# Kernel tuning notes

Hardware: AMD Instinct MI355X
Metric: run time of the kernel (lower is better)

The kernel has to match this reference:

```python
import jax, jax.numpy as jnp
import numpy as np

HEAD_DIM = 32
KERNEL = 3
DILATION = 2
SCALE = HEAD_DIM ** -0.5


def _unfold(x, kernel, dilation):
    # x: [B, C, H, W] -> patches [B, C, kernel*kernel, H, W]
    # matches nn.Unfold(kernel, dilation, padding=dilation*(kernel-1)//2, stride=1)
    B, C, H, W = x.shape
    pad = dilation * (kernel - 1) // 2
    xp = jnp.pad(x, ((0, 0), (0, 0), (pad, pad), (pad, pad)))
    patches = jnp.stack(
        [xp[:, :, i * dilation:i * dilation + H, j * dilation:j * dilation + W]
         for i in range(kernel) for j in range(kernel)],
        axis=2,
    )
    return patches  # [B, C, k*k, H, W]


def setup_inputs() -> dict:
    key = jax.random.key(0)
    kq, kk, kv = jax.random.split(key, 3)
    shape = (8, 192, 56, 56)
    return {
        "q": jax.random.normal(kq, shape, dtype=jnp.float32),
        "k": jax.random.normal(kk, shape, dtype=jnp.float32),
        "v": jax.random.normal(kv, shape, dtype=jnp.float32),
    }


def reference(q, k, v):
    B, d, H, W = q.shape
    h = d // HEAD_DIM
    kk2 = KERNEL * KERNEL
    HW = H * W

    # q: [B, h, hd, HW]
    qh = q.reshape(B, h, HEAD_DIM, HW)
    # unfolded k/v: [B, h, hd, k*k, HW]
    kp = _unfold(k, KERNEL, DILATION).reshape(B, h, HEAD_DIM, kk2, HW)
    vp = _unfold(v, KERNEL, DILATION).reshape(B, h, HEAD_DIM, kk2, HW)

    attn = jnp.einsum('bhdn,bhdkn->bhnk', qh, kp) * SCALE
    attn = jax.nn.softmax(attn, axis=-1)
    # dropout p=0 (eval): no-op

    # [B, h, HW, hd]
    out = jnp.einsum('bhnk,bhdkn->bhnd', attn, vp)
    # transpose(1,2).reshape(B,H,W,d): channel order = head-major
    out = out.transpose(0, 2, 1, 3).reshape(B, H, W, d)
    return out
```

## Files before the change

### kernel.cpp

```cpp
#include <hip/hip_runtime.h>

#define BATCH 8
#define NH 6
#define HEAD_DIM 32
#define CCH 192
#define HH 56
#define WW 56
#define HWSZ (HH * WW)
#define KPOS 9
#define SCALE 0.17677669529663687f

__global__ __launch_bounds__(256) void dilate_attn_kernel(
    const float* __restrict__ q,
    const float* __restrict__ k,
    const float* __restrict__ v,
    float* __restrict__ out)
{
    int tid = blockIdx.x * blockDim.x + threadIdx.x;
    if (tid >= BATCH * NH * HWSZ) return;

    int x  = tid % WW;
    int y  = (tid / WW) % HH;
    int bh = tid / HWSZ;
    int h  = bh % NH;
    int b  = bh / NH;

    const size_t chan_base = (size_t)(b * CCH + h * HEAD_DIM) * HWSZ;
    const float* qb = q + chan_base + y * WW + x;
    const float* kb = k + chan_base;
    const float* vb = v + chan_base;

    int  off[KPOS];
    bool ok[KPOS];
#pragma unroll
    for (int kk = 0; kk < KPOS; kk++) {
        int yy = y + 2 * (kk / 3) - 2;
        int xx = x + 2 * (kk % 3) - 2;
        bool good = (yy >= 0) & (yy < HH) & (xx >= 0) & (xx < WW);
        ok[kk]  = good;
        off[kk] = good ? (yy * WW + xx) : 0;
    }

    float attn[KPOS];
#pragma unroll
    for (int kk = 0; kk < KPOS; kk++) attn[kk] = 0.0f;

#pragma unroll 4
    for (int d = 0; d < HEAD_DIM; d++) {
        float qd = qb[(size_t)d * HWSZ];
        const float* kd = kb + (size_t)d * HWSZ;
#pragma unroll
        for (int kk = 0; kk < KPOS; kk++) {
            float kval = ok[kk] ? kd[off[kk]] : 0.0f;
            attn[kk] = fmaf(qd, kval, attn[kk]);
        }
    }

    float m = attn[0] * SCALE;
#pragma unroll
    for (int kk = 0; kk < KPOS; kk++) {
        attn[kk] *= SCALE;
        m = fmaxf(m, attn[kk]);
    }
    float s = 0.0f;
#pragma unroll
    for (int kk = 0; kk < KPOS; kk++) {
        attn[kk] = __expf(attn[kk] - m);
        s += attn[kk];
    }
    float inv = 1.0f / s;
#pragma unroll
    for (int kk = 0; kk < KPOS; kk++) attn[kk] *= inv;

    float* ob = out + ((size_t)((b * HH + y) * WW + x)) * CCH + h * HEAD_DIM;

#pragma unroll 2
    for (int d4 = 0; d4 < HEAD_DIM; d4 += 4) {
        float4 acc = make_float4(0.f, 0.f, 0.f, 0.f);
        const float* vd = vb + (size_t)d4 * HWSZ;
#pragma unroll
        for (int kk = 0; kk < KPOS; kk++) {
            if (ok[kk]) {
                const float* vp = vd + off[kk];
                acc.x = fmaf(attn[kk], vp[0 * HWSZ], acc.x);
                acc.y = fmaf(attn[kk], vp[1 * HWSZ], acc.y);
                acc.z = fmaf(attn[kk], vp[2 * HWSZ], acc.z);
                acc.w = fmaf(attn[kk], vp[3 * HWSZ], acc.w);
            }
        }
        *reinterpret_cast<float4*>(ob + d4) = acc;
    }
}

extern "C" void kernel_launch(void* const* d_in, const int* in_sizes, int n_in,
                              void* d_out, int out_size, void* d_ws, size_t ws_size,
                              hipStream_t stream) {
    const float* q = (const float*)d_in[0];
    const float* k = (const float*)d_in[1];
    const float* v = (const float*)d_in[2];
    float* out = (float*)d_out;

    const int total = BATCH * NH * HWSZ;
    const int block = 256;
    const int grid  = (total + block - 1) / block;
    dilate_attn_kernel<<<grid, block, 0, stream>>>(q, k, v, out);
}
```

Before: 129.3 us.

## Repack K/V into zero-padded channel-last planes and vectorize tap loads

Adds a repack kernel that transposes K and V into a zero-padded [bh, 60, 60, 32] channel-last layout in workspace. The main kernel can then read each tap's 32 channels as contiguous float4 loads without bounds checks. It also preloads q into registers. This replaces strided per-channel gathers with vectorized loads, at the cost of an extra kernel launch and a full write and reread of K and V through global memory.

```diff
diff --git a/kernel.cpp b/kernel.cpp
--- a/kernel.cpp
+++ b/kernel.cpp
@@ -7,61 +7,96 @@
 #define HH 56
 #define WW 56
 #define HWSZ (HH * WW)
+#define PH 60
+#define PW 60
+#define PPLANE (PH * PW)
 #define KPOS 9
 #define SCALE 0.17677669529663687f
 
-__global__ __launch_bounds__(256) void dilate_attn_kernel(
+__global__ __launch_bounds__(256) void repack_kernel(
+    const float* __restrict__ k, const float* __restrict__ v,
+    float* __restrict__ kp, float* __restrict__ vp)
+{
+    __shared__ float lds[HEAD_DIM * 57];
+
+    int yy = blockIdx.x % PH;
+    int bh = blockIdx.x / PH;
+    const float* src = (blockIdx.y == 0) ? k : v;
+    float*       dst = (blockIdx.y == 0) ? kp : vp;
+
+    int t = threadIdx.x;
+    bool interior_row = (yy >= 2) && (yy < 58);
+
+    if (interior_row) {
+        int y = yy - 2;
+        const float* s = src + (size_t)bh * (HEAD_DIM * HWSZ) + y * WW;
+#pragma unroll
+        for (int i = 0; i < 7; i++) {
+            int idx = t + i * 256;
+            int d = idx / WW;
+            int x = idx - d * WW;
+            lds[d * 57 + x] = s[d * HWSZ + x];
+        }
+    }
+    __syncthreads();
+
+    float* drow = dst + ((size_t)bh * PPLANE + (size_t)yy * PW) * HEAD_DIM;
+#pragma unroll
+    for (int i = 0; i < 8; i++) {
+        int idx = t + i * 256;
+        if (idx < PW * HEAD_DIM) {
+            int xx = idx >> 5;
+            int d  = idx & 31;
+            float val = 0.0f;
+            if (interior_row && xx >= 2 && xx < 58)
+                val = lds[d * 57 + (xx - 2)];
+            drow[idx] = val;
+        }
+    }
+}
+
+__global__ __launch_bounds__(256) void dilate_attn_main(
     const float* __restrict__ q,
-    const float* __restrict__ k,
-    const float* __restrict__ v,
+    const float* __restrict__ kp,
+    const float* __restrict__ vp,
     float* __restrict__ out)
 {
-    int tid = blockIdx.x * blockDim.x + threadIdx.x;
-    if (tid >= BATCH * NH * HWSZ) return;
-
+    int tid = blockIdx.x * 256 + threadIdx.x;
     int x  = tid % WW;
     int y  = (tid / WW) % HH;
     int bh = tid / HWSZ;
-    int h  = bh % NH;
-    int b  = bh / NH;
 
-    const size_t chan_base = (size_t)(b * CCH + h * HEAD_DIM) * HWSZ;
-    const float* qb = q + chan_base + y * WW + x;
-    const float* kb = k + chan_base;
-    const float* vb = v + chan_base;
+    const float* qb = q + (size_t)bh * (HEAD_DIM * HWSZ) + y * WW + x;
+    float qreg[HEAD_DIM];
+#pragma unroll
+    for (int d = 0; d < HEAD_DIM; d++) qreg[d] = qb[d * HWSZ];
 
-    int  off[KPOS];
-    bool ok[KPOS];
+    int tap[KPOS];
 #pragma unroll
     for (int kk = 0; kk < KPOS; kk++) {
-        int yy = y + 2 * (kk / 3) - 2;
-        int xx = x + 2 * (kk % 3) - 2;
-        bool good = (yy >= 0) & (yy < HH) & (xx >= 0) & (xx < WW);
-        ok[kk]  = good;
-        off[kk] = good ? (yy * WW + xx) : 0;
+        int iy = kk / 3, ix = kk % 3;
+        tap[kk] = (bh * PPLANE + (y + 2 * iy) * PW + (x + 2 * ix)) * HEAD_DIM;
     }
 
     float attn[KPOS];
 #pragma unroll
-    for (int kk = 0; kk < KPOS; kk++) attn[kk] = 0.0f;
-
-#pragma unroll 4
-    for (int d = 0; d < HEAD_DIM; d++) {
-        float qd = qb[(size_t)d * HWSZ];
-        const float* kd = kb + (size_t)d * HWSZ;
+    for (int kk = 0; kk < KPOS; kk++) {
+        const float4* kt = reinterpret_cast<const float4*>(kp + tap[kk]);
+        float acc = 0.0f;
 #pragma unroll
-        for (int kk = 0; kk < KPOS; kk++) {
-            float kval = ok[kk] ? kd[off[kk]] : 0.0f;
-            attn[kk] = fmaf(qd, kval, attn[kk]);
+        for (int j = 0; j < 8; j++) {
+            float4 kv = kt[j];
+            acc = fmaf(qreg[4 * j + 0], kv.x, acc);
+            acc = fmaf(qreg[4 * j + 1], kv.y, acc);
+            acc = fmaf(qreg[4 * j + 2], kv.z, acc);
+            acc = fmaf(qreg[4 * j + 3], kv.w, acc);
         }
+        attn[kk] = acc * SCALE;
     }
 
-    float m = attn[0] * SCALE;
+    float m = attn[0];
 #pragma unroll
-    for (int kk = 0; kk < KPOS; kk++) {
-        attn[kk] *= SCALE;
-        m = fmaxf(m, attn[kk]);
-    }
+    for (int kk = 1; kk < KPOS; kk++) m = fmaxf(m, attn[kk]);
     float s = 0.0f;
 #pragma unroll
     for (int kk = 0; kk < KPOS; kk++) {
@@ -72,24 +107,30 @@
 #pragma unroll
     for (int kk = 0; kk < KPOS; kk++) attn[kk] *= inv;
 
+    float4 acc[8];
+#pragma unroll
+    for (int j = 0; j < 8; j++) acc[j] = make_float4(0.f, 0.f, 0.f, 0.f);
+
+#pragma unroll
+    for (int kk = 0; kk < KPOS; kk++) {
+        const float4* vt = reinterpret_cast<const float4*>(vp + tap[kk]);
+        float a = attn[kk];
+#pragma unroll
+        for (int j = 0; j < 8; j++) {
+            float4 vv = vt[j];
+            acc[j].x = fmaf(a, vv.x, acc[j].x);
+            acc[j].y = fmaf(a, vv.y, acc[j].y);
+            acc[j].z = fmaf(a, vv.z, acc[j].z);
+            acc[j].w = fmaf(a, vv.w, acc[j].w);
+        }
+    }
+
+    int h = bh % NH;
+    int b = bh / NH;
     float* ob = out + ((size_t)((b * HH + y) * WW + x)) * CCH + h * HEAD_DIM;
-
-#pragma unroll 2
-    for (int d4 = 0; d4 < HEAD_DIM; d4 += 4) {
-        float4 acc = make_float4(0.f, 0.f, 0.f, 0.f);
-        const float* vd = vb + (size_t)d4 * HWSZ;
+    float4* ob4 = reinterpret_cast<float4*>(ob);
 #pragma unroll
-        for (int kk = 0; kk < KPOS; kk++) {
-            if (ok[kk]) {
-                const float* vp = vd + off[kk];
-                acc.x = fmaf(attn[kk], vp[0 * HWSZ], acc.x);
-                acc.y = fmaf(attn[kk], vp[1 * HWSZ], acc.y);
-                acc.z = fmaf(attn[kk], vp[2 * HWSZ], acc.z);
-                acc.w = fmaf(attn[kk], vp[3 * HWSZ], acc.w);
-            }
-        }
-        *reinterpret_cast<float4*>(ob + d4) = acc;
-    }
+    for (int j = 0; j < 8; j++) ob4[j] = acc[j];
 }
 
 extern "C" void kernel_launch(void* const* d_in, const int* in_sizes, int n_in,
@@ -100,8 +141,13 @@
     const float* v = (const float*)d_in[2];
     float* out = (float*)d_out;
 
+    const size_t plane_elems = (size_t)BATCH * NH * PPLANE * HEAD_DIM;
+    float* kp = (float*)d_ws;
+    float* vp = kp + plane_elems;
+
+    dim3 rgrid(BATCH * NH * PH, 2);
+    repack_kernel<<<rgrid, 256, 0, stream>>>(k, v, kp, vp);
+
     const int total = BATCH * NH * HWSZ;
-    const int block = 256;
-    const int grid  = (total + block - 1) / block;
-    dilate_attn_kernel<<<grid, block, 0, stream>>>(q, k, v, out);
+    dilate_attn_main<<<total / 256, 256, 0, stream>>>(q, kp, vp, out);
 }
```

After: 184.1 us. 42.5% more time.

## Split QK and AV phases across threads with shared-memory attention weights

Applied to the files above, without the earlier changes.

Each block now handles 64 pixels with 256 threads. In the first phase, threads are assigned per pixel and kernel row (3 rows, so 192 active threads), and each computes three dot products. The resulting scores go to shared memory. In the second phase, 4 threads per pixel each compute softmax and accumulate 8 output channels over the 9 neighbours. This raises parallelism per pixel and spreads the V gathers and stores across more threads, which helps latency hiding. The cost is a block barrier, a quarter of threads idle in phase one, and softmax computed redundantly by all four threads of each pixel.

```diff
diff --git a/kernel.cpp b/kernel.cpp
--- a/kernel.cpp
+++ b/kernel.cpp
@@ -1,6 +1,5 @@
 #include <hip/hip_runtime.h>
 
-#define BATCH 8
 #define NH 6
 #define HEAD_DIM 32
 #define CCH 192
@@ -9,86 +8,105 @@
 #define HWSZ (HH * WW)
 #define KPOS 9
 #define SCALE 0.17677669529663687f
+#define PXB 64
 
-__global__ __launch_bounds__(256) void dilate_attn_kernel(
+__global__ __launch_bounds__(256) void dilate_attn_fused(
     const float* __restrict__ q,
     const float* __restrict__ k,
     const float* __restrict__ v,
     float* __restrict__ out)
 {
-    int tid = blockIdx.x * blockDim.x + threadIdx.x;
-    if (tid >= BATCH * NH * HWSZ) return;
+    __shared__ float sattn[PXB * 13];
+    const int t = threadIdx.x;
 
-    int x  = tid % WW;
-    int y  = (tid / WW) % HH;
-    int bh = tid / HWSZ;
-    int h  = bh % NH;
-    int b  = bh / NH;
+    {
+        const int iy = t >> 6;
+        const int pl = t & 63;
+        if (iy < 3) {
+            const int gp = blockIdx.x * PXB + pl;
+            const int x  = gp % WW;
+            const int y  = (gp / WW) % HH;
+            const int bh = gp / HWSZ;
+            const int yy = y + 2 * iy - 2;
 
-    const size_t chan_base = (size_t)(b * CCH + h * HEAD_DIM) * HWSZ;
-    const float* qb = q + chan_base + y * WW + x;
-    const float* kb = k + chan_base;
-    const float* vb = v + chan_base;
-
-    int  off[KPOS];
-    bool ok[KPOS];
+            float a0 = 0.f, a1 = 0.f, a2 = 0.f;
+            if (yy >= 0 && yy < HH) {
+                const float* qb = q + (size_t)bh * (HEAD_DIM * HWSZ) + y * WW + x;
+                const float* kb = k + (size_t)bh * (HEAD_DIM * HWSZ) + yy * WW;
+                const bool ok0 = (x - 2) >= 0;
+                const bool ok2 = (x + 2) < WW;
+                const int  o0  = ok0 ? (x - 2) : 0;
+                const int  o1  = x;
+                const int  o2  = ok2 ? (x + 2) : 0;
 #pragma unroll
-    for (int kk = 0; kk < KPOS; kk++) {
-        int yy = y + 2 * (kk / 3) - 2;
-        int xx = x + 2 * (kk % 3) - 2;
-        bool good = (yy >= 0) & (yy < HH) & (xx >= 0) & (xx < WW);
-        ok[kk]  = good;
-        off[kk] = good ? (yy * WW + xx) : 0;
-    }
-
-    float attn[KPOS];
-#pragma unroll
-    for (int kk = 0; kk < KPOS; kk++) attn[kk] = 0.0f;
-
-#pragma unroll 4
-    for (int d = 0; d < HEAD_DIM; d++) {
-        float qd = qb[(size_t)d * HWSZ];
-        const float* kd = kb + (size_t)d * HWSZ;
-#pragma unroll
-        for (int kk = 0; kk < KPOS; kk++) {
-            float kval = ok[kk] ? kd[off[kk]] : 0.0f;
-            attn[kk] = fmaf(qd, kval, attn[kk]);
+                for (int d = 0; d < HEAD_DIM; d++) {
+                    const float qd = qb[d * HWSZ];
+                    const float* kd = kb + d * HWSZ;
+                    a0 = fmaf(qd, kd[o0], a0);
+                    a1 = fmaf(qd, kd[o1], a1);
+                    a2 = fmaf(qd, kd[o2], a2);
+                }
+                if (!ok0) a0 = 0.f;
+                if (!ok2) a2 = 0.f;
+            }
+            sattn[pl * 13 + iy * 3 + 0] = a0 * SCALE;
+            sattn[pl * 13 + iy * 3 + 1] = a1 * SCALE;
+            sattn[pl * 13 + iy * 3 + 2] = a2 * SCALE;
         }
     }
 
-    float m = attn[0] * SCALE;
+    __syncthreads();
+
+    {
+        const int pl = t >> 2;
+        const int dq = t & 3;
+        const int gp = blockIdx.x * PXB + pl;
+        const int x  = gp % WW;
+        const int y  = (gp / WW) % HH;
+        const int bh = gp / HWSZ;
+
+        float a[KPOS];
 #pragma unroll
-    for (int kk = 0; kk < KPOS; kk++) {
-        attn[kk] *= SCALE;
-        m = fmaxf(m, attn[kk]);
-    }
-    float s = 0.0f;
+        for (int kk = 0; kk < KPOS; kk++) a[kk] = sattn[pl * 13 + kk];
+
+        float m = a[0];
 #pragma unroll
-    for (int kk = 0; kk < KPOS; kk++) {
-        attn[kk] = __expf(attn[kk] - m);
-        s += attn[kk];
-    }
-    float inv = 1.0f / s;
-#pragma unroll
-    for (int kk = 0; kk < KPOS; kk++) attn[kk] *= inv;
-
-    float* ob = out + ((size_t)((b * HH + y) * WW + x)) * CCH + h * HEAD_DIM;
-
-#pragma unroll 2
-    for (int d4 = 0; d4 < HEAD_DIM; d4 += 4) {
-        float4 acc = make_float4(0.f, 0.f, 0.f, 0.f);
-        const float* vd = vb + (size_t)d4 * HWSZ;
+        for (int kk = 1; kk < KPOS; kk++) m = fmaxf(m, a[kk]);
+        float s = 0.f;
 #pragma unroll
         for (int kk = 0; kk < KPOS; kk++) {
-            if (ok[kk]) {
-                const float* vp = vd + off[kk];
-                acc.x = fmaf(attn[kk], vp[0 * HWSZ], acc.x);
-                acc.y = fmaf(attn[kk], vp[1 * HWSZ], acc.y);
-                acc.z = fmaf(attn[kk], vp[2 * HWSZ], acc.z);
-                acc.w = fmaf(attn[kk], vp[3 * HWSZ], acc.w);
-            }
+            a[kk] = __expf(a[kk] - m);
+            s += a[kk];
         }
-        *reinterpret_cast<float4*>(ob + d4) = acc;
+        const float inv = 1.f / s;
+
+        const float* vb = v + (size_t)bh * (HEAD_DIM * HWSZ) + (size_t)dq * 8 * HWSZ;
+
+        float acc[8];
+#pragma unroll
+        for (int j = 0; j < 8; j++) acc[j] = 0.f;
+
+#pragma unroll
+        for (int kk = 0; kk < KPOS; kk++) {
+            const int yy = y + 2 * (kk / 3) - 2;
+            const int xx = x + 2 * (kk % 3) - 2;
+            const bool ok = (yy >= 0) & (yy < HH) & (xx >= 0) & (xx < WW);
+            const int off = ok ? (yy * WW + xx) : 0;
+            const float w = ok ? (a[kk] * inv) : 0.f;
+            const float* vp = vb + off;
+#pragma unroll
+            for (int j = 0; j < 8; j++)
+                acc[j] = fmaf(w, vp[j * HWSZ], acc[j]);
+        }
+
+        const int h = bh % NH;
+        const int b = bh / NH;
+        float* ob = out + ((size_t)((b * HH + y) * WW + x)) * CCH
+                        + h * HEAD_DIM + dq * 8;
+        float4 r0 = make_float4(acc[0], acc[1], acc[2], acc[3]);
+        float4 r1 = make_float4(acc[4], acc[5], acc[6], acc[7]);
+        reinterpret_cast<float4*>(ob)[0] = r0;
+        reinterpret_cast<float4*>(ob)[1] = r1;
     }
 }
 
@@ -100,8 +118,7 @@
     const float* v = (const float*)d_in[2];
     float* out = (float*)d_out;
 
-    const int total = BATCH * NH * HWSZ;
-    const int block = 256;
-    const int grid  = (total + block - 1) / block;
-    dilate_attn_kernel<<<grid, block, 0, stream>>>(q, k, v, out);
+    const int total_px = 8 * NH * HWSZ;
+    const int blocks = total_px / PXB;
+    dilate_attn_fused<<<blocks, 256, 0, stream>>>(q, k, v, out);
 }
```

After: 123.9 us. 4.1% less time.

## Split head dimension across 8 lanes per pixel with shuffle reduction

Applied to the files above, without the earlier changes.

Each pixel is now handled by 8 lanes, each owning 4 head channels, which gives 8x more threads. The q·k partial dot products are summed with xor shuffles, and softmax is computed redundantly in every lane. Out-of-bounds neighbours now use a float mask and a clamped offset instead of branches, and each lane writes one float4 of the output. This raises parallelism and memory-level parallelism, but coalescing changes because the 8 lanes of a pixel read different channel planes, so a wavefront covers only 8 pixels per plane.

```diff
diff --git a/kernel.cpp b/kernel.cpp
--- a/kernel.cpp
+++ b/kernel.cpp
@@ -1,6 +1,5 @@
 #include <hip/hip_runtime.h>
 
-#define BATCH 8
 #define NH 6
 #define HEAD_DIM 32
 #define CCH 192
@@ -10,86 +9,85 @@
 #define KPOS 9
 #define SCALE 0.17677669529663687f
 
-__global__ __launch_bounds__(256) void dilate_attn_kernel(
+__global__ __launch_bounds__(256, 4) void dilate_attn_v4(
     const float* __restrict__ q,
     const float* __restrict__ k,
     const float* __restrict__ v,
     float* __restrict__ out)
 {
-    int tid = blockIdx.x * blockDim.x + threadIdx.x;
-    if (tid >= BATCH * NH * HWSZ) return;
+    const int tid = blockIdx.x * 256 + threadIdx.x;
+    const int l   = tid & 7;
+    const int p   = tid >> 3;
+    const int x   = p % WW;
+    const int y   = (p / WW) % HH;
+    const int bh  = p / HWSZ;
 
-    int x  = tid % WW;
-    int y  = (tid / WW) % HH;
-    int bh = tid / HWSZ;
-    int h  = bh % NH;
-    int b  = bh / NH;
+    const size_t dbase = ((size_t)bh * HEAD_DIM + 4 * l) * HWSZ;
 
-    const size_t chan_base = (size_t)(b * CCH + h * HEAD_DIM) * HWSZ;
-    const float* qb = q + chan_base + y * WW + x;
-    const float* kb = k + chan_base;
-    const float* vb = v + chan_base;
+    const float* qb = q + dbase + y * WW + x;
+    const float q0 = qb[0];
+    const float q1 = qb[HWSZ];
+    const float q2 = qb[2 * HWSZ];
+    const float q3 = qb[3 * HWSZ];
 
-    int  off[KPOS];
-    bool ok[KPOS];
+    const float* kb = k + dbase;
+    const float* vb = v + dbase;
+
+    int   off[KPOS];
+    float msk[KPOS];
 #pragma unroll
     for (int kk = 0; kk < KPOS; kk++) {
-        int yy = y + 2 * (kk / 3) - 2;
-        int xx = x + 2 * (kk % 3) - 2;
-        bool good = (yy >= 0) & (yy < HH) & (xx >= 0) & (xx < WW);
-        ok[kk]  = good;
-        off[kk] = good ? (yy * WW + xx) : 0;
+        const int yy = y + 2 * (kk / 3) - 2;
+        const int xx = x + 2 * (kk % 3) - 2;
+        const bool ok = (yy >= 0) & (yy < HH) & (xx >= 0) & (xx < WW);
+        off[kk] = ok ? (yy * WW + xx) : (y * WW + x);
+        msk[kk] = ok ? 1.0f : 0.0f;
     }
 
-    float attn[KPOS];
+    float lg[KPOS];
 #pragma unroll
-    for (int kk = 0; kk < KPOS; kk++) attn[kk] = 0.0f;
-
-#pragma unroll 4
-    for (int d = 0; d < HEAD_DIM; d++) {
-        float qd = qb[(size_t)d * HWSZ];
-        const float* kd = kb + (size_t)d * HWSZ;
-#pragma unroll
-        for (int kk = 0; kk < KPOS; kk++) {
-            float kval = ok[kk] ? kd[off[kk]] : 0.0f;
-            attn[kk] = fmaf(qd, kval, attn[kk]);
-        }
+    for (int kk = 0; kk < KPOS; kk++) {
+        const float* kp = kb + off[kk];
+        float pa =        q0 * kp[0];
+        pa = fmaf(q1, kp[HWSZ],     pa);
+        pa = fmaf(q2, kp[2 * HWSZ], pa);
+        pa = fmaf(q3, kp[3 * HWSZ], pa);
+        pa += __shfl_xor(pa, 1);
+        pa += __shfl_xor(pa, 2);
+        pa += __shfl_xor(pa, 4);
+        lg[kk] = pa * SCALE * msk[kk];
     }
 
-    float m = attn[0] * SCALE;
+    float m = lg[0];
+#pragma unroll
+    for (int kk = 1; kk < KPOS; kk++) m = fmaxf(m, lg[kk]);
+    float s = 0.0f;
+    float w[KPOS];
 #pragma unroll
     for (int kk = 0; kk < KPOS; kk++) {
-        attn[kk] *= SCALE;
-        m = fmaxf(m, attn[kk]);
+        w[kk] = __expf(lg[kk] - m);
+        s += w[kk];
     }
-    float s = 0.0f;
+    const float inv = 1.0f / s;
+#pragma unroll
+    for (int kk = 0; kk < KPOS; kk++) w[kk] *= inv * msk[kk];
+
+    float a0 = 0.f, a1 = 0.f, a2 = 0.f, a3 = 0.f;
 #pragma unroll
     for (int kk = 0; kk < KPOS; kk++) {
-        attn[kk] = __expf(attn[kk] - m);
-        s += attn[kk];
+        const float* vp = vb + off[kk];
+        const float wk = w[kk];
+        a0 = fmaf(wk, vp[0],         a0);
+        a1 = fmaf(wk, vp[HWSZ],      a1);
+        a2 = fmaf(wk, vp[2 * HWSZ],  a2);
+        a3 = fmaf(wk, vp[3 * HWSZ],  a3);
     }
-    float inv = 1.0f / s;
-#pragma unroll
-    for (int kk = 0; kk < KPOS; kk++) attn[kk] *= inv;
 
-    float* ob = out + ((size_t)((b * HH + y) * WW + x)) * CCH + h * HEAD_DIM;
-
-#pragma unroll 2
-    for (int d4 = 0; d4 < HEAD_DIM; d4 += 4) {
-        float4 acc = make_float4(0.f, 0.f, 0.f, 0.f);
-        const float* vd = vb + (size_t)d4 * HWSZ;
-#pragma unroll
-        for (int kk = 0; kk < KPOS; kk++) {
-            if (ok[kk]) {
-                const float* vp = vd + off[kk];
-                acc.x = fmaf(attn[kk], vp[0 * HWSZ], acc.x);
-                acc.y = fmaf(attn[kk], vp[1 * HWSZ], acc.y);
-                acc.z = fmaf(attn[kk], vp[2 * HWSZ], acc.z);
-                acc.w = fmaf(attn[kk], vp[3 * HWSZ], acc.w);
-            }
-        }
-        *reinterpret_cast<float4*>(ob + d4) = acc;
-    }
+    const int h = bh % NH;
+    const int b = bh / NH;
+    float* ob = out + ((size_t)((b * HH + y) * WW + x)) * CCH
+                    + h * HEAD_DIM + 4 * l;
+    *reinterpret_cast<float4*>(ob) = make_float4(a0, a1, a2, a3);
 }
 
 extern "C" void kernel_launch(void* const* d_in, const int* in_sizes, int n_in,
@@ -100,8 +98,6 @@
     const float* v = (const float*)d_in[2];
     float* out = (float*)d_out;
 
-    const int total = BATCH * NH * HWSZ;
-    const int block = 256;
-    const int grid  = (total + block - 1) / block;
-    dilate_attn_kernel<<<grid, block, 0, stream>>>(q, k, v, out);
+    const int blocks = (8 * NH * HWSZ * 8) / 256;
+    dilate_attn_v4<<<blocks, 256, 0, stream>>>(q, k, v, out);
 }
```

After: 164.5 us. 27.2% more time.
